# Kernel optimization log

Hardware: AMD Instinct MI355X
Metric: run time of the kernel (lower is better)

The kernel has to match this reference:

```python
import jax, jax.numpy as jnp
import numpy as np

B, S, D, H = 2, 2048, 1024, 16
DK = D // H


def setup_inputs() -> dict:
    key = jax.random.key(0)
    ks = jax.random.split(key, 9)
    sc = 0.02
    return {
        "x": jax.random.normal(ks[0], (B, S, D), dtype=jnp.float32),
        "attention_mask": jnp.ones((B, S), dtype=jnp.int32),
        "Wq": jax.random.normal(ks[1], (D, D), dtype=jnp.float32) * sc,
        "bq": jax.random.normal(ks[2], (D,), dtype=jnp.float32) * sc,
        "Wk": jax.random.normal(ks[3], (D, D), dtype=jnp.float32) * sc,
        "bk": jax.random.normal(ks[4], (D,), dtype=jnp.float32) * sc,
        "Wv": jax.random.normal(ks[5], (D, D), dtype=jnp.float32) * sc,
        "bv": jax.random.normal(ks[6], (D,), dtype=jnp.float32) * sc,
        "Wo": jax.random.normal(ks[7], (D, D), dtype=jnp.float32) * sc,
        "bo": jax.random.normal(ks[8], (D,), dtype=jnp.float32) * sc,
    }


def reference(x, attention_mask, Wq, bq, Wk, bk, Wv, bv, Wo, bo):
    b, s, d = x.shape
    # projections (Linear: x @ W + b) then split heads -> [b, h, s, dk]
    def heads(t):
        return t.reshape(b, s, H, DK).transpose(0, 2, 1, 3)
    Q = heads(x @ Wq + bq)
    K = heads(x @ Wk + bk)
    V = heads(x @ Wv + bv)
    # NOTE: original computes K @ Q^T (not Q @ K^T) and applies NO 1/sqrt(dk) scale
    scores = jnp.einsum("bhid,bhjd->bhij", K, Q)  # [b, h, s, s]
    causal = jnp.tril(jnp.ones((s, s), dtype=bool))  # [s, s]
    final_mask = attention_mask[:, None, None, :].astype(bool) & causal[None, None]
    scores = jnp.where(final_mask, scores, -jnp.inf)
    attn = jax.nn.softmax(scores, axis=-1)
    out = jnp.einsum("bhij,bhjd->bhid", attn, V)  # [b, h, s, dk]
    out = out.transpose(0, 2, 1, 3).reshape(b, s, d)
    return out @ Wo + bo
```

## Files before the change

kernel.cpp:

```cpp
#include <hip/hip_runtime.h>
#include <stdint.h>
#include <stddef.h>


typedef short bf16x8 __attribute__((ext_vector_type(8)));
typedef float f32x4  __attribute__((ext_vector_type(4)));

__device__ __forceinline__ short f2bf(float f) {
  union { float f; uint32_t u; } a; a.f = f;
  uint32_t r = a.u + 0x7fffu + ((a.u >> 16) & 1u);
  return (short)(r >> 16);
}
__device__ __forceinline__ float bf2f(short s) {
  union { uint32_t u; float f; } a; a.u = ((uint32_t)(uint16_t)s) << 16;
  return a.f;
}
__device__ __forceinline__ uint32_t pack2bf(float a, float b) {
  union { float f; uint32_t u; } x, y; x.f = a; y.f = b;
  return (x.u >> 16) | (y.u & 0xffff0000u);
}
__device__ __forceinline__ float fast_exp2(float x) {
#if __has_builtin(__builtin_amdgcn_exp2f)
  return __builtin_amdgcn_exp2f(x);
#else
  return exp2f(x);
#endif
}
__device__ __forceinline__ void async16(const void* g, void* l) {
  __builtin_amdgcn_global_load_lds(
      (const __attribute__((address_space(1))) uint32_t*)g,
      (__attribute__((address_space(3))) uint32_t*)l, 16, 0, 0);
}
#define MFMA(a, b, c) __builtin_amdgcn_mfma_f32_16x16x32_bf16((a), (b), (c), 0, 0, 0)

__global__ void k_split_x(const float* __restrict__ x, short* __restrict__ xhi) {
  int i = blockIdx.x * 256 + threadIdx.x;
  float4 v = ((const float4*)x)[i];
  short4 h;
  h.x = f2bf(v.x);
  h.y = f2bf(v.y);
  h.z = f2bf(v.z);
  h.w = f2bf(v.w);
  ((short4*)xhi)[i] = h;
}

__global__ void k_prep_w(const float* __restrict__ Wq, const float* __restrict__ Wk,
                         const float* __restrict__ Wv, const float* __restrict__ Wo,
                         short* __restrict__ whi, short* __restrict__ wo) {
  __shared__ float T[64][65];
  int z = blockIdx.z;
  const float* W = (z == 0) ? Wq : (z == 1) ? Wk : (z == 2) ? Wv : Wo;
  int n0 = blockIdx.x * 64, k0 = blockIdx.y * 64;
  int t = threadIdx.x;
  int rr = t >> 4, cc = (t & 15) * 4;
#pragma unroll
  for (int it = 0; it < 4; ++it) {
    int row = rr + it * 16;
    float4 v = *(const float4*)&W[(size_t)(k0 + row) * 1024 + n0 + cc];
    T[row][cc] = v.x; T[row][cc + 1] = v.y; T[row][cc + 2] = v.z; T[row][cc + 3] = v.w;
  }
  __syncthreads();
  short* oh = (z < 3) ? (whi + (size_t)z * 1048576) : wo;
#pragma unroll
  for (int it = 0; it < 4; ++it) {
    int nrow = rr + it * 16;
    short4 h4;
    h4.x = f2bf(T[cc + 0][nrow]);
    h4.y = f2bf(T[cc + 1][nrow]);
    h4.z = f2bf(T[cc + 2][nrow]);
    h4.w = f2bf(T[cc + 3][nrow]);
    *(short4*)&oh[(size_t)(n0 + nrow) * 1024 + k0 + cc] = h4;
  }
}

__global__ __launch_bounds__(256, 3) void k_gemm_qkv(
    const short* __restrict__ xhi, const short* __restrict__ whi,
    const float* __restrict__ bq, const float* __restrict__ bk,
    const float* __restrict__ bv,
    short* __restrict__ Qhi, short* __restrict__ Qlo,
    short* __restrict__ Khi, short* __restrict__ Klo,
    short* __restrict__ Vt) {
  __shared__ short AH[2][4096];
  __shared__ short BH[2][4096];
  int tid = threadIdx.x;
  int bx = blockIdx.x;
  int m0 = blockIdx.y * 128;
  int n0g = bx * 128;
  int w = tid >> 6, lane = tid & 63, lr = lane & 15, lq = lane >> 4;
  int wm = w >> 1, wn = w & 1;
  int z = bx >> 3;
  f32x4 acc[4][4] = {};

  auto stage = [&](int ks, int pb) {
#pragma unroll
    for (int it = 0; it < 2; ++it) {
      int idx = it * 256 + tid;
      int row = idx >> 2, c = idx & 3;
      int cs = c ^ (row & 3);
      async16(xhi + (size_t)(m0 + row) * 1024 + ks * 32 + cs * 8, &AH[pb][idx * 8]);
      async16(whi + (size_t)(n0g + row) * 1024 + ks * 32 + cs * 8, &BH[pb][idx * 8]);
    }
  };

  stage(0, 0);
  int p = 0;
  int g = lq ^ (lr & 3);
  if (z == 2) {
    for (int ks = 0; ks < 32; ++ks) {
      __syncthreads();
      if (ks < 31) stage(ks + 1, p ^ 1);
      const bf16x8* A8 = (const bf16x8*)AH[p];
      const bf16x8* B8 = (const bf16x8*)BH[p];
      bf16x8 af[4], bfr[4];
#pragma unroll
      for (int mt = 0; mt < 4; ++mt) af[mt] = A8[(wm * 64 + mt * 16 + lr) * 4 + g];
#pragma unroll
      for (int nt = 0; nt < 4; ++nt) bfr[nt] = B8[(wn * 64 + nt * 16 + lr) * 4 + g];
#pragma unroll
      for (int mt = 0; mt < 4; ++mt)
#pragma unroll
        for (int nt = 0; nt < 4; ++nt)
          acc[mt][nt] = MFMA(af[mt], bfr[nt], acc[mt][nt]);
      p ^= 1;
    }
#pragma unroll
    for (int nt = 0; nt < 4; ++nt) {
      int dg = (n0g & 1023) + wn * 64 + nt * 16 + lr;
      float bvv = bv[dg];
      int hh = dg >> 6, dk = dg & 63;
#pragma unroll
      for (int mt = 0; mt < 4; ++mt) {
        int row = m0 + wm * 64 + mt * 16 + lq * 4;
        int b_ = row >> 11, s_ = row & 2047;
        short4 pk;
        pk.x = f2bf(acc[mt][nt][0] + bvv);
        pk.y = f2bf(acc[mt][nt][1] + bvv);
        pk.z = f2bf(acc[mt][nt][2] + bvv);
        pk.w = f2bf(acc[mt][nt][3] + bvv);
        *(short4*)&Vt[(size_t)((b_ * 16 + hh) * 64 + dk) * 2048 + s_] = pk;
      }
    }
  } else {
    for (int ks = 0; ks < 32; ++ks) {
      __syncthreads();
      if (ks < 31) stage(ks + 1, p ^ 1);
      const bf16x8* A8 = (const bf16x8*)AH[p];
      const bf16x8* B8 = (const bf16x8*)BH[p];
      bf16x8 af[4], bfr[4];
#pragma unroll
      for (int mt = 0; mt < 4; ++mt) af[mt] = A8[(wm * 64 + mt * 16 + lr) * 4 + g];
#pragma unroll
      for (int nt = 0; nt < 4; ++nt) bfr[nt] = B8[(wn * 64 + nt * 16 + lr) * 4 + g];
#pragma unroll
      for (int mt = 0; mt < 4; ++mt)
#pragma unroll
        for (int nt = 0; nt < 4; ++nt)
          acc[mt][nt] = MFMA(bfr[nt], af[mt], acc[mt][nt]);
      p ^= 1;
    }
    const float LOG2E = 1.44269504f;
    const float* bias = (z == 0) ? bq : bk;
    short* Ch = (z == 0) ? Qhi : Khi;
    short* Cl = (z == 0) ? Qlo : Klo;
#pragma unroll
    for (int mt = 0; mt < 4; ++mt) {
      int row = m0 + wm * 64 + mt * 16 + lr;
#pragma unroll
      for (int nt = 0; nt < 4; ++nt) {
        int colg = (n0g & 1023) + wn * 64 + nt * 16 + lq * 4;
        float4 b4 = *(const float4*)&bias[colg];
        float v0 = acc[mt][nt][0] + b4.x;
        float v1 = acc[mt][nt][1] + b4.y;
        float v2 = acc[mt][nt][2] + b4.z;
        float v3 = acc[mt][nt][3] + b4.w;
        if (z == 0) { v0 *= LOG2E; v1 *= LOG2E; v2 *= LOG2E; v3 *= LOG2E; }
        short4 hi4, lo4;
        hi4.x = f2bf(v0); lo4.x = f2bf(v0 - bf2f(hi4.x));
        hi4.y = f2bf(v1); lo4.y = f2bf(v1 - bf2f(hi4.y));
        hi4.z = f2bf(v2); lo4.z = f2bf(v2 - bf2f(hi4.z));
        hi4.w = f2bf(v3); lo4.w = f2bf(v3 - bf2f(hi4.w));
        size_t o = (size_t)row * 1024 + colg;
        *(short4*)&Ch[o] = hi4;
        if (z == 1) *(short4*)&Cl[o] = lo4;
      }
    }
  }
}

__global__ __launch_bounds__(256, 3) void k_gemm_o(
    const short* __restrict__ Ab, const short* __restrict__ Bb,
    const float* __restrict__ bias, float* __restrict__ Cf) {
  __shared__ short AH[2][4096];
  __shared__ short BH[2][4096];
  int tid = threadIdx.x;
  int m0 = blockIdx.y * 128, n0 = blockIdx.x * 128;
  int w = tid >> 6, lane = tid & 63, lr = lane & 15, lq = lane >> 4;
  int wm = w >> 1, wn = w & 1;
  f32x4 acc[4][4] = {};

  auto stage = [&](int ks, int pb) {
#pragma unroll
    for (int it = 0; it < 2; ++it) {
      int idx = it * 256 + tid;
      int row = idx >> 2, c = idx & 3;
      int cs = c ^ (row & 3);
      async16(Ab + (size_t)(m0 + row) * 1024 + ks * 32 + cs * 8, &AH[pb][idx * 8]);
      async16(Bb + (size_t)(n0 + row) * 1024 + ks * 32 + cs * 8, &BH[pb][idx * 8]);
    }
  };

  stage(0, 0);
  int p = 0;
  int g = lq ^ (lr & 3);
  for (int ks = 0; ks < 32; ++ks) {
    __syncthreads();
    if (ks < 31) stage(ks + 1, p ^ 1);
    const bf16x8* A8 = (const bf16x8*)AH[p];
    const bf16x8* B8 = (const bf16x8*)BH[p];
    bf16x8 af[4], bfr[4];
#pragma unroll
    for (int mt = 0; mt < 4; ++mt) af[mt] = A8[(wm * 64 + mt * 16 + lr) * 4 + g];
#pragma unroll
    for (int nt = 0; nt < 4; ++nt) bfr[nt] = B8[(wn * 64 + nt * 16 + lr) * 4 + g];
#pragma unroll
    for (int mt = 0; mt < 4; ++mt)
#pragma unroll
      for (int nt = 0; nt < 4; ++nt)
        acc[mt][nt] = MFMA(bfr[nt], af[mt], acc[mt][nt]);
    p ^= 1;
  }

#pragma unroll
  for (int mt = 0; mt < 4; ++mt) {
    int row = m0 + wm * 64 + mt * 16 + lr;
#pragma unroll
    for (int nt = 0; nt < 4; ++nt) {
      int colg = n0 + wn * 64 + nt * 16 + lq * 4;
      float4 b4 = *(const float4*)&bias[colg];
      float4 o4;
      o4.x = acc[mt][nt][0] + b4.x;
      o4.y = acc[mt][nt][1] + b4.y;
      o4.z = acc[mt][nt][2] + b4.z;
      o4.w = acc[mt][nt][3] + b4.w;
      *(float4*)&Cf[(size_t)row * 1024 + colg] = o4;
    }
  }
}

__global__ __launch_bounds__(256, 4) void k_attn(
    const short* __restrict__ Khi, const short* __restrict__ Klo,
    const short* __restrict__ Qhi, const short* __restrict__ Qlo,
    const short* __restrict__ Vt, const int* __restrict__ amask,
    short* __restrict__ Obuf) {
  __shared__ short QH[2][4096];
  __shared__ short VS[2][4096];
  int tid = threadIdx.x;
  int bid = blockIdx.x;
  int xcd = bid & 7, idx = bid >> 3;
  int bh = xcd * 4 + (idx & 3);
  int L  = 32 - (idx >> 2);
  int b = bh >> 4, h = bh & 15;
  int w = tid >> 6, lane = tid & 63, lr = lane & 15, lq = lane >> 4;
  int band = 2 * (L - 1) + (w >> 1);
  int rb0 = band * 32 + (w & 1) * 16;

  bf16x8 kh[2], kl[2];
  {
    size_t ra = ((size_t)(b * 2048 + rb0 + lr)) * 1024 + h * 64;
#pragma unroll
    for (int ks = 0; ks < 2; ++ks) {
      kh[ks] = *(const bf16x8*)(Khi + ra + ks * 32 + lq * 8);
      kl[ks] = *(const bf16x8*)(Klo + ra + ks * 32 + lq * 8);
    }
  }

  f32x4 O[4] = {};
  float ls = 0.f;
  int iq = rb0 + lr;
  int baddr0 = (((lq & 1) * 2) * 16 + lr) * 4;
  int baddr1 = baddr0 + 64;

  auto stage = [&](int jt, int pb) {
    int j0 = jt * 64;
#pragma unroll
    for (int it = 0; it < 2; ++it) {
      int idx2 = it * 256 + tid;
      int rr = idx2 >> 3, c = idx2 & 7;
      int cs = c ^ (rr & 7);
      size_t gq = ((size_t)(b * 2048 + j0 + rr)) * 1024 + h * 64 + cs * 8;
      async16(Qhi + gq, &QH[pb][idx2 * 8]);
      size_t gv = ((size_t)(bh * 64 + rr)) * 2048 + j0 + cs * 8;
      async16(Vt + gv, &VS[pb][idx2 * 8]);
    }
  };

  stage(0, 0);
  int p = 0;
  for (int t = 0; t < L; ++t) {
    __syncthreads();
    if (t + 1 < L) stage(t + 1, p ^ 1);
    int j0 = t * 64;
    const bf16x8* Q8 = (const bf16x8*)QH[p];
    const bf16x8* V8 = (const bf16x8*)VS[p];

    int av = amask[b * 2048 + j0 + lane];
    unsigned long long bal = __ballot(av != 0);
    bool allv = (bal == ~0ull);

    f32x4 s[4] = {};
#pragma unroll
    for (int mt = 0; mt < 4; ++mt) {
      int row = mt * 16 + lr;
#pragma unroll
      for (int ks = 0; ks < 2; ++ks) {
        int gi = row * 8 + ((ks * 4 + lq) ^ (row & 7));
        bf16x8 qa = Q8[gi];
        s[mt] = MFMA(qa, kh[ks], s[mt]);
        s[mt] = MFMA(qa, kl[ks], s[mt]);
      }
    }

    bool diag = (t == L - 1);
    float pv[4][4];
#pragma unroll
    for (int mt = 0; mt < 4; ++mt)
#pragma unroll
      for (int r = 0; r < 4; ++r)
        pv[mt][r] = fast_exp2(s[mt][r]);
    if (diag) {
#pragma unroll
      for (int mt = 0; mt < 4; ++mt)
#pragma unroll
        for (int r = 0; r < 4; ++r)
          if (j0 + mt * 16 + lq * 4 + r > iq) pv[mt][r] = 0.f;
    }
    if (!allv) {
#pragma unroll
      for (int mt = 0; mt < 4; ++mt)
#pragma unroll
        for (int r = 0; r < 4; ++r)
          if (!((bal >> (mt * 16 + lq * 4 + r)) & 1)) pv[mt][r] = 0.f;
    }
    uint32_t pd[4][2];
#pragma unroll
    for (int mt = 0; mt < 4; ++mt) {
      ls += (pv[mt][0] + pv[mt][1]) + (pv[mt][2] + pv[mt][3]);
      pd[mt][0] = pack2bf(pv[mt][0], pv[mt][1]);
      pd[mt][1] = pack2bf(pv[mt][2], pv[mt][3]);
    }

#pragma unroll
    for (int k2 = 0; k2 < 2; ++k2) {
      union { int i[4]; bf16x8 v; } pa;
#pragma unroll
      for (int dd = 0; dd < 4; ++dd) {
        int addr = (dd >> 1) ? baddr1 : baddr0;
        int v0 = __builtin_amdgcn_ds_bpermute(addr, (int)pd[k2 * 2 + 0][dd & 1]);
        int v1 = __builtin_amdgcn_ds_bpermute(addr, (int)pd[k2 * 2 + 1][dd & 1]);
        pa.i[dd] = (lq >> 1) ? v1 : v0;
      }
#pragma unroll
      for (int nt = 0; nt < 4; ++nt) {
        int row = nt * 16 + lr;
        bf16x8 vb = V8[row * 8 + ((k2 * 4 + lq) ^ (row & 7))];
        O[nt] = MFMA(pa.v, vb, O[nt]);
      }
    }
    p ^= 1;
  }

  float tsum = ls;
  tsum += __shfl_xor(tsum, 16);
  tsum += __shfl_xor(tsum, 32);
  float inv[4];
#pragma unroll
  for (int r = 0; r < 4; ++r) inv[r] = 1.0f / __shfl(tsum, lq * 4 + r, 64);
#pragma unroll
  for (int nt = 0; nt < 4; ++nt)
#pragma unroll
    for (int r = 0; r < 4; ++r) {
      int row = b * 2048 + rb0 + lq * 4 + r;
      int col = h * 64 + nt * 16 + lr;
      Obuf[(size_t)row * 1024 + col] = f2bf(O[nt][r] * inv[r]);
    }
}

extern "C" void kernel_launch(void* const* d_in, const int* in_sizes, int n_in,
                              void* d_out, int out_size, void* d_ws, size_t ws_size,
                              hipStream_t stream) {
  const float* x  = (const float*)d_in[0];
  const int* amask = (const int*)d_in[1];
  const float* Wq = (const float*)d_in[2];
  const float* bq = (const float*)d_in[3];
  const float* Wk = (const float*)d_in[4];
  const float* bk = (const float*)d_in[5];
  const float* Wv = (const float*)d_in[6];
  const float* bv = (const float*)d_in[7];
  const float* Wo = (const float*)d_in[8];
  const float* bo = (const float*)d_in[9];

  char* ws = (char*)d_ws;
  const size_t MB = 1024 * 1024;
  short* xhi = (short*)(ws);
  short* whi = (short*)(ws + 16 * MB);
  short* wo  = (short*)(ws + 26 * MB);
  short* Qhi = (short*)(ws + 28 * MB);
  short* Qlo = (short*)(ws + 36 * MB);
  short* Khi = (short*)(ws + 44 * MB);
  short* Klo = (short*)(ws + 52 * MB);
  short* Vt  = (short*)(ws + 60 * MB);
  short* Obuf = xhi;

  k_split_x<<<4096, 256, 0, stream>>>(x, xhi);
  k_prep_w<<<dim3(16, 16, 4), 256, 0, stream>>>(Wq, Wk, Wv, Wo, whi, wo);

  k_gemm_qkv<<<dim3(24, 32), 256, 0, stream>>>(xhi, whi, bq, bk, bv,
                                               Qhi, Qlo, Khi, Klo, Vt);
  k_attn<<<1024, 256, 0, stream>>>(Khi, Klo, Qhi, Qlo, Vt, amask, Obuf);
  k_gemm_o<<<dim3(8, 32), 256, 0, stream>>>(Obuf, wo, bo, (float*)d_out);
}
```

Measured before the change: 206.8 us.

## Split long causal attention rows into two partial blocks and merge

```diff
diff --git a/kernel.cpp b/kernel.cpp
--- a/kernel.cpp
+++ b/kernel.cpp
@@ -249,19 +249,32 @@
 
 __global__ __launch_bounds__(256, 4) void k_attn(
     const short* __restrict__ Khi, const short* __restrict__ Klo,
-    const short* __restrict__ Qhi, const short* __restrict__ Qlo,
-    const short* __restrict__ Vt, const int* __restrict__ amask,
-    short* __restrict__ Obuf) {
+    const short* __restrict__ Qhi, const short* __restrict__ Vt,
+    const int* __restrict__ amask, short* __restrict__ Obuf,
+    float* __restrict__ PA, float* __restrict__ PB,
+    float* __restrict__ LA, float* __restrict__ LB) {
   __shared__ short QH[2][4096];
   __shared__ short VS[2][4096];
   int tid = threadIdx.x;
   int bid = blockIdx.x;
-  int xcd = bid & 7, idx = bid >> 3;
-  int bh = xcd * 4 + (idx & 3);
-  int L  = 32 - (idx >> 2);
+  int xcd = bid & 7, i2 = bid >> 3;
+  int bh = xcd * 4 + (i2 & 3);
+  int o  = i2 >> 2;
+  int P, t0, t1;
+  bool partial, slotB = false;
+  if (o < 16) {
+    P = 16 + o; t0 = 0; t1 = 16; partial = true;
+  } else {
+    int q = o - 16, lvl = q >> 1;
+    if (q & 1) {
+      P = 15 - lvl; t0 = 0; t1 = P + 1; partial = false;
+    } else {
+      P = 31 - lvl; t0 = 16; t1 = P + 1; partial = true; slotB = true;
+    }
+  }
   int b = bh >> 4, h = bh & 15;
   int w = tid >> 6, lane = tid & 63, lr = lane & 15, lq = lane >> 4;
-  int band = 2 * (L - 1) + (w >> 1);
+  int band = 2 * P + (w >> 1);
   int rb0 = band * 32 + (w & 1) * 16;
 
   bf16x8 kh[2], kl[2];
@@ -294,11 +307,11 @@
     }
   };
 
-  stage(0, 0);
+  stage(t0, 0);
   int p = 0;
-  for (int t = 0; t < L; ++t) {
+  for (int t = t0; t < t1; ++t) {
     __syncthreads();
-    if (t + 1 < L) stage(t + 1, p ^ 1);
+    if (t + 1 < t1) stage(t + 1, p ^ 1);
     int j0 = t * 64;
     const bf16x8* Q8 = (const bf16x8*)QH[p];
     const bf16x8* V8 = (const bf16x8*)VS[p];
@@ -320,7 +333,7 @@
       }
     }
 
-    bool diag = (t == L - 1);
+    bool diag = (t == P);
     float pv[4][4];
 #pragma unroll
     for (int mt = 0; mt < 4; ++mt)
@@ -372,17 +385,49 @@
   float tsum = ls;
   tsum += __shfl_xor(tsum, 16);
   tsum += __shfl_xor(tsum, 32);
-  float inv[4];
-#pragma unroll
-  for (int r = 0; r < 4; ++r) inv[r] = 1.0f / __shfl(tsum, lq * 4 + r, 64);
-#pragma unroll
-  for (int nt = 0; nt < 4; ++nt)
-#pragma unroll
-    for (int r = 0; r < 4; ++r) {
-      int row = b * 2048 + rb0 + lq * 4 + r;
-      int col = h * 64 + nt * 16 + lr;
-      Obuf[(size_t)row * 1024 + col] = f2bf(O[nt][r] * inv[r]);
-    }
+
+  if (!partial) {
+    float inv[4];
+#pragma unroll
+    for (int r = 0; r < 4; ++r) inv[r] = 1.0f / __shfl(tsum, lq * 4 + r, 64);
+#pragma unroll
+    for (int nt = 0; nt < 4; ++nt)
+#pragma unroll
+      for (int r = 0; r < 4; ++r) {
+        int row = b * 2048 + rb0 + lq * 4 + r;
+        int col = h * 64 + nt * 16 + lr;
+        Obuf[(size_t)row * 1024 + col] = f2bf(O[nt][r] * inv[r]);
+      }
+  } else {
+    float* PO = slotB ? PB : PA;
+    float* PL = slotB ? LB : LA;
+    int prb = bh * 1024 + (P - 16) * 64 + w * 16;
+#pragma unroll
+    for (int nt = 0; nt < 4; ++nt)
+#pragma unroll
+      for (int r = 0; r < 4; ++r)
+        PO[(size_t)(prb + lq * 4 + r) * 64 + nt * 16 + lr] = O[nt][r];
+    if (lq == 0) PL[prb + lr] = tsum;
+  }
+}
+
+__global__ void k_merge(const float* __restrict__ PA, const float* __restrict__ PB,
+                        const float* __restrict__ LA, const float* __restrict__ LB,
+                        short* __restrict__ Obuf) {
+  int t = blockIdx.x * 256 + threadIdx.x;
+  int pr = t >> 4, cg = t & 15;
+  float4 a = ((const float4*)PA)[pr * 16 + cg];
+  float4 bb4 = ((const float4*)PB)[pr * 16 + cg];
+  float inv = 1.0f / (LA[pr] + LB[pr]);
+  int bh = pr >> 10, P = 16 + ((pr >> 6) & 15), loc = pr & 63;
+  int b = bh >> 4, h = bh & 15;
+  size_t addr = ((size_t)(b * 2048 + P * 64 + loc)) * 1024 + h * 64 + cg * 4;
+  short4 oq;
+  oq.x = f2bf((a.x + bb4.x) * inv);
+  oq.y = f2bf((a.y + bb4.y) * inv);
+  oq.z = f2bf((a.z + bb4.z) * inv);
+  oq.w = f2bf((a.w + bb4.w) * inv);
+  *(short4*)&Obuf[addr] = oq;
 }
 
 extern "C" void kernel_launch(void* const* d_in, const int* in_sizes, int n_in,
@@ -402,9 +447,13 @@
   char* ws = (char*)d_ws;
   const size_t MB = 1024 * 1024;
   short* xhi = (short*)(ws);
+  float* PA  = (float*)(ws + 8 * MB);
   short* whi = (short*)(ws + 16 * MB);
+  float* LA  = (float*)(ws + 22 * MB);
+  float* LB  = (float*)(ws + 23 * MB);
   short* wo  = (short*)(ws + 26 * MB);
   short* Qhi = (short*)(ws + 28 * MB);
+  float* PB  = (float*)(ws + 36 * MB);
   short* Qlo = (short*)(ws + 36 * MB);
   short* Khi = (short*)(ws + 44 * MB);
   short* Klo = (short*)(ws + 52 * MB);
@@ -416,6 +465,8 @@
 
   k_gemm_qkv<<<dim3(24, 32), 256, 0, stream>>>(xhi, whi, bq, bk, bv,
                                                Qhi, Qlo, Khi, Klo, Vt);
-  k_attn<<<1024, 256, 0, stream>>>(Khi, Klo, Qhi, Qlo, Vt, amask, Obuf);
+  k_attn<<<1536, 256, 0, stream>>>(Khi, Klo, Qhi, Vt, amask, Obuf,
+                                   PA, PB, LA, LB);
+  k_merge<<<2048, 256, 0, stream>>>(PA, PB, LA, LB, Obuf);
   k_gemm_o<<<dim3(8, 32), 256, 0, stream>>>(Obuf, wo, bo, (float*)d_out);
 }
```

After: 202.5 us. -2.1%, faster.
